# Kernel tuning notes

Measured on AMD Instinct MI355X. Metric: run time of the kernel, lower is better.

The kernel has to match this reference:

```python
import jax, jax.numpy as jnp
import numpy as np

EMBED = 128
N_RBF = 8


def setup_inputs() -> dict:
    key = jax.random.key(0)
    ks = jax.random.split(key, 12)
    n_edges = 640000
    num_atoms = 10000
    s = 1.0 / np.sqrt(EMBED)
    inp = {
        "m_ji": jax.random.normal(ks[0], (n_edges, EMBED), dtype=jnp.float32),
        "e_rbf": jax.random.normal(ks[1], (n_edges, N_RBF), dtype=jnp.float32),
        "nbr_list": jax.random.randint(ks[2], (n_edges, 2), 0, num_atoms, dtype=jnp.int32),
        "num_atoms": num_atoms,
        # params (torch Linear stores W as [out, in]; we keep that convention)
        "W_edge": jax.random.normal(ks[3], (EMBED, N_RBF), dtype=jnp.float32) / np.sqrt(N_RBF),
        "W1": jax.random.normal(ks[4], (EMBED, EMBED), dtype=jnp.float32) * s,
        "b1": jnp.zeros((EMBED,), dtype=jnp.float32),
        "W2": jax.random.normal(ks[5], (EMBED, EMBED), dtype=jnp.float32) * s,
        "b2": jnp.zeros((EMBED,), dtype=jnp.float32),
        "W3": jax.random.normal(ks[6], (EMBED, EMBED), dtype=jnp.float32) * s,
        "b3": jnp.zeros((EMBED,), dtype=jnp.float32),
        "W_final": jax.random.normal(ks[7], (EMBED, EMBED), dtype=jnp.float32) * s,
    }
    return inp


def reference(m_ji, e_rbf, nbr_list, num_atoms, W_edge, W1, b1, W2, b2, W3, b3, W_final):
    # edge_linear(e_rbf) * m_ji  -> [n_edges, embed]
    prod = (e_rbf @ W_edge.T) * m_ji
    # scatter_add over receiving atom index -> [num_atoms, embed]
    node_feats = jax.ops.segment_sum(prod, nbr_list[:, 0], num_segments=num_atoms)
    # 3 dense layers with swish (SiLU) activation
    for W, b in ((W1, b1), (W2, b2), (W3, b3)):
        node_feats = jax.nn.silu(node_feats @ W.T + b)
    # final linear (no bias)
    return node_feats @ W_final.T
```

## Files before the change

kernel.cpp:

```cpp
#include <hip/hip_runtime.h>

#define EMBED 128
#define NRBF 8
#define CAP 160

typedef __attribute__((ext_vector_type(8))) short bf16x8;
typedef __attribute__((ext_vector_type(4))) float f32x4;

static __device__ __forceinline__ unsigned short f2bf(float f) {
  unsigned u = __builtin_bit_cast(unsigned, f);
  u = (u + 0x7fffu + ((u >> 16) & 1u)) >> 16;
  return (unsigned short)u;
}

static __device__ __forceinline__ float silu_f(float x) {
  return x / (1.0f + __expf(-x));
}

__global__ __launch_bounds__(256) void prep_kernel(
    const float* __restrict__ W1, const float* __restrict__ W2,
    const float* __restrict__ W3, const float* __restrict__ Wf,
    const float* __restrict__ b1, const float* __restrict__ b2,
    const float* __restrict__ b3,
    unsigned short* __restrict__ Wbf, float* __restrict__ bws,
    unsigned* __restrict__ cursor, int num_atoms)
{
  int i = blockIdx.x * 256 + threadIdx.x;
  if (i < 16384) {
    Wbf[i]         = f2bf(W1[i]);
    Wbf[16384 + i] = f2bf(W2[i]);
    Wbf[32768 + i] = f2bf(W3[i]);
    Wbf[49152 + i] = f2bf(Wf[i]);
  }
  if (i < 128) {
    bws[i] = b1[i]; bws[128 + i] = b2[i]; bws[256 + i] = b3[i];
  }
  if (i < num_atoms) cursor[i] = 0u;
}

__global__ __launch_bounds__(256) void bucket_kernel(
    const int* __restrict__ nbr, unsigned* __restrict__ cursor,
    int* __restrict__ sorted, int n_edges)
{
  int i = blockIdx.x * blockDim.x + threadIdx.x;
  const int stride = gridDim.x * blockDim.x;
  const int2* nb = reinterpret_cast<const int2*>(nbr);
  for (; i < n_edges; i += stride) {
    const int dst = nb[i].x;
    unsigned pos = atomicAdd(&cursor[dst], 1u);
    if (pos < CAP) sorted[(size_t)dst * CAP + pos] = i;
  }
}

__global__ __launch_bounds__(256) void gather_kernel(
    const float* __restrict__ m_ji, const float* __restrict__ e_rbf,
    const int* __restrict__ sorted, const unsigned* __restrict__ cnts,
    const float* __restrict__ W_edge, unsigned short* __restrict__ node_bf,
    int num_atoms)
{
  const int lane = threadIdx.x & 63;
  const int li = lane & 31;
  const int half = lane >> 5;
  const int wid = blockIdx.x * (blockDim.x >> 6) + (threadIdx.x >> 6);
  if (wid >= num_atoms) return;

  f32x4 wT[NRBF];
#pragma unroll
  for (int k = 0; k < NRBF; ++k) {
#pragma unroll
    for (int q = 0; q < 4; ++q) wT[k][q] = W_edge[(li * 4 + q) * NRBF + k];
  }

  int cnt = (int)cnts[wid];
  if (cnt > CAP) cnt = CAP;
  const int* sb = sorted + (size_t)wid * CAP;
  const char* mbase = (const char*)m_ji;
  const char* rbase = (const char*)e_rbf;
  const unsigned moff_lane = (unsigned)(li * 16);

  f32x4 acc = {0.f, 0.f, 0.f, 0.f};

  for (int base = 0; base < cnt; base += 64) {
    const int rem = min(64, cnt - base);
    const int myeid = (base + lane < cnt) ? sb[base + lane] : sb[base];
#pragma unroll 4
    for (int j = 0; j < rem; j += 2) {
      const int idx = j + half;
      const float vm = (idx < rem) ? 1.0f : 0.0f;
      const int eid = __shfl(myeid, idx & 63);
      const unsigned mo = ((unsigned)eid << 9) + moff_lane;
      const unsigned ro = (unsigned)eid << 5;
      const f32x4 m4 = *reinterpret_cast<const f32x4*>(mbase + mo);
      const f32x4 r0 = *reinterpret_cast<const f32x4*>(rbase + ro);
      const f32x4 r1 = *reinterpret_cast<const f32x4*>(rbase + ro + 16);

      f32x4 p = wT[0] * r0.x;
      p += wT[1] * r0.y;
      p += wT[2] * r0.z;
      p += wT[3] * r0.w;
      p += wT[4] * r1.x;
      p += wT[5] * r1.y;
      p += wT[6] * r1.z;
      p += wT[7] * r1.w;
      p *= vm;
      acc += p * m4;
    }
  }

  acc[0] += __shfl_xor(acc[0], 32);
  acc[1] += __shfl_xor(acc[1], 32);
  acc[2] += __shfl_xor(acc[2], 32);
  acc[3] += __shfl_xor(acc[3], 32);

  if (half == 0) {
    unsigned u0 = (unsigned)f2bf(acc[0]) | ((unsigned)f2bf(acc[1]) << 16);
    unsigned u1 = (unsigned)f2bf(acc[2]) | ((unsigned)f2bf(acc[3]) << 16);
    uint2 v = {u0, u1};
    *reinterpret_cast<uint2*>(node_bf + (size_t)wid * EMBED + li * 4) = v;
  }
}

__global__ __launch_bounds__(256) void mlp_mfma_kernel(
    const unsigned short* __restrict__ node_bf,
    const unsigned short* __restrict__ Wbf,
    const float* __restrict__ bws,
    float* __restrict__ out, int num_atoms)
{
  __shared__ unsigned short x_lds[64 * 128];
  char* xb = (char*)x_lds;
  const int lane = threadIdx.x & 63;
  const int wave = threadIdx.x >> 6;
  const int rbase = blockIdx.x * 64;

#pragma unroll
  for (int it = 0; it < 4; ++it) {
    int i = it * 64 + lane;
    int r = i >> 4;
    int s = i & 15;
    int row = wave * 16 + r;
    int grow = rbase + row;
    uint4 v = {0u, 0u, 0u, 0u};
    if (grow < num_atoms)
      v = *reinterpret_cast<const uint4*>(node_bf + (size_t)grow * 128 + s * 8);
    *reinterpret_cast<uint4*>(xb + row * 256 + ((s ^ (row & 7)) * 16)) = v;
  }

  const int arow = wave * 16 + (lane & 15);
  const int kb = lane >> 4;
  const int colbase = lane & 15;

  f32x4 acc[8];
#pragma unroll
  for (int layer = 0; layer < 4; ++layer) {
    const unsigned short* W = Wbf + layer * 16384;
#pragma unroll
    for (int t = 0; t < 8; ++t) {
      if (layer < 3) {
        float bv = bws[layer * 128 + t * 16 + colbase];
        acc[t] = (f32x4){bv, bv, bv, bv};
      } else {
        acc[t] = (f32x4){0.f, 0.f, 0.f, 0.f};
      }
    }
#pragma unroll
    for (int ks = 0; ks < 4; ++ks) {
      bf16x8 a = *reinterpret_cast<const bf16x8*>(
          xb + arow * 256 + (((ks * 4 + kb) ^ (arow & 7)) * 16));
#pragma unroll
      for (int t = 0; t < 8; ++t) {
        int col = t * 16 + colbase;
        bf16x8 b = *reinterpret_cast<const bf16x8*>(W + col * 128 + ks * 32 + kb * 8);
        acc[t] = __builtin_amdgcn_mfma_f32_16x16x32_bf16(a, b, acc[t], 0, 0, 0);
      }
    }
    if (layer < 3) {
#pragma unroll
      for (int t = 0; t < 8; ++t) {
        int col = t * 16 + colbase;
        int s = col >> 3;
        int cw = (col & 7) * 2;
#pragma unroll
        for (int j = 0; j < 4; ++j) {
          int row = wave * 16 + (lane >> 4) * 4 + j;
          unsigned short h = f2bf(silu_f(acc[t][j]));
          *reinterpret_cast<unsigned short*>(
              xb + row * 256 + ((s ^ (row & 7)) * 16) + cw) = h;
        }
      }
    } else {
#pragma unroll
      for (int t = 0; t < 8; ++t) {
        int col = t * 16 + colbase;
#pragma unroll
        for (int j = 0; j < 4; ++j) {
          int row = wave * 16 + (lane >> 4) * 4 + j;
          int grow = rbase + row;
          if (grow < num_atoms) out[(size_t)grow * 128 + col] = acc[t][j];
        }
      }
    }
  }
}

extern "C" void kernel_launch(void* const* d_in, const int* in_sizes, int n_in,
                              void* d_out, int out_size, void* d_ws, size_t ws_size,
                              hipStream_t stream) {
  const float* m_ji   = (const float*)d_in[0];
  const float* e_rbf  = (const float*)d_in[1];
  const int*   nbr    = (const int*)d_in[2];
  const float* W_edge = (const float*)d_in[4];
  const float* W1 = (const float*)d_in[5];
  const float* b1 = (const float*)d_in[6];
  const float* W2 = (const float*)d_in[7];
  const float* b2 = (const float*)d_in[8];
  const float* W3 = (const float*)d_in[9];
  const float* b3 = (const float*)d_in[10];
  const float* Wf = (const float*)d_in[11];
  float* out = (float*)d_out;

  const int n_edges   = in_sizes[0] / EMBED;
  const int num_atoms = out_size / EMBED;

  auto align256 = [](size_t x) { return (x + 255) & ~(size_t)255; };
  char* p = (char*)d_ws;
  unsigned short* node_bf = (unsigned short*)p;
  p += align256((size_t)num_atoms * EMBED * sizeof(unsigned short));
  unsigned* cursor    = (unsigned*)p;  p += align256((size_t)num_atoms * 4);
  int* sorted         = (int*)p;       p += align256((size_t)num_atoms * CAP * 4);
  unsigned short* Wbf = (unsigned short*)p; p += align256((size_t)4 * 128 * 128 * 2);
  float* bws          = (float*)p;     p += align256((size_t)3 * 128 * 4);

  prep_kernel<<<64, 256, 0, stream>>>(W1, W2, W3, Wf, b1, b2, b3, Wbf, bws,
                                      cursor, num_atoms);

  bucket_kernel<<<1024, 256, 0, stream>>>(nbr, cursor, sorted, n_edges);

  const int gblocks = (num_atoms + 3) / 4;
  gather_kernel<<<gblocks, 256, 0, stream>>>(m_ji, e_rbf, sorted, cursor,
                                             W_edge, node_bf, num_atoms);

  const int mlp_blocks = (num_atoms + 63) / 64;
  mlp_mfma_kernel<<<mlp_blocks, 256, 0, stream>>>(node_bf, Wbf, bws, out, num_atoms);
}
```

Before: 154.7 us.

## Stream edges coalesced into per-atom bf16 payload buckets, then reduce per atom

Replaces the index-bucketing plus random gather of m_ji rows with a kernel that reads edges sequentially, computes the edge product, and writes it as bf16 into a per-destination slot claimed by atomicAdd. A second kernel reduces each atom's bucket into node features. The aim is to turn scattered 512-byte row gathers into coalesced streaming reads. In exchange it writes and rereads an intermediate of about 200 MB of bf16 workspace, quantizes each edge product to bf16 before summation, and falls back to the old path when the workspace is too small.

After: 175.4 us. 1.13x slower.

```diff
diff --git a/kernel.cpp b/kernel.cpp
--- a/kernel.cpp
+++ b/kernel.cpp
@@ -38,6 +38,96 @@
   if (i < num_atoms) cursor[i] = 0u;
 }
 
+__global__ __launch_bounds__(256) void edge_stream_kernel(
+    const float* __restrict__ m_ji, const float* __restrict__ e_rbf,
+    const int* __restrict__ nbr, const float* __restrict__ W_edge,
+    unsigned* __restrict__ cursor, unsigned short* __restrict__ payload,
+    int n_edges)
+{
+  const int lane = threadIdx.x & 63;
+  const int li = lane & 31;
+  const int half = lane >> 5;
+  const int wid = blockIdx.x * (blockDim.x >> 6) + (threadIdx.x >> 6);
+  const int n_waves = gridDim.x * (blockDim.x >> 6);
+
+  f32x4 wT[NRBF];
+#pragma unroll
+  for (int k = 0; k < NRBF; ++k) {
+#pragma unroll
+    for (int q = 0; q < 4; ++q) wT[k][q] = W_edge[(li * 4 + q) * NRBF + k];
+  }
+
+  for (int e0 = wid * 2; e0 < n_edges; e0 += n_waves * 2) {
+    const int e = e0 + half;
+    const bool act = (e < n_edges);
+    f32x4 m4 = {0.f, 0.f, 0.f, 0.f};
+    if (act) m4 = reinterpret_cast<const f32x4*>(m_ji)[(size_t)e0 * 32 + lane];
+    f32x4 r0 = {0.f, 0.f, 0.f, 0.f}, r1 = r0;
+    int dst = 0;
+    if (act) {
+      r0 = reinterpret_cast<const f32x4*>(e_rbf)[(size_t)e * 2];
+      r1 = reinterpret_cast<const f32x4*>(e_rbf)[(size_t)e * 2 + 1];
+      dst = nbr[2 * e];
+    }
+    int pos = 0;
+    if (li == 0 && act) pos = (int)atomicAdd(&cursor[dst], 1u);
+    pos = __shfl(pos, lane & 32);
+
+    f32x4 p = wT[0] * r0.x;
+    p += wT[1] * r0.y;
+    p += wT[2] * r0.z;
+    p += wT[3] * r0.w;
+    p += wT[4] * r1.x;
+    p += wT[5] * r1.y;
+    p += wT[6] * r1.z;
+    p += wT[7] * r1.w;
+    p *= m4;
+
+    if (act && pos < CAP) {
+      unsigned u0 = (unsigned)f2bf(p[0]) | ((unsigned)f2bf(p[1]) << 16);
+      unsigned u1 = (unsigned)f2bf(p[2]) | ((unsigned)f2bf(p[3]) << 16);
+      char* rowp = (char*)payload + ((size_t)dst * CAP + pos) * 256 + li * 8;
+      *reinterpret_cast<uint2*>(rowp) = (uint2){u0, u1};
+    }
+  }
+}
+
+__global__ __launch_bounds__(256) void reduce_kernel(
+    const unsigned short* __restrict__ payload,
+    const unsigned* __restrict__ cnts,
+    unsigned short* __restrict__ node_bf, int num_atoms)
+{
+  const int lane = threadIdx.x & 63;
+  const int wid = blockIdx.x * (blockDim.x >> 6) + (threadIdx.x >> 6);
+  if (wid >= num_atoms) return;
+
+  int cnt = (int)cnts[wid];
+  if (cnt > CAP) cnt = CAP;
+  const unsigned* base =
+      reinterpret_cast<const unsigned*>(payload + (size_t)wid * CAP * 128) + lane;
+
+  float a0 = 0.f, a1 = 0.f;
+  int r = 0;
+  for (; r + 8 <= cnt; r += 8) {
+    unsigned u[8];
+#pragma unroll
+    for (int k = 0; k < 8; ++k) u[k] = base[(r + k) * 64];
+#pragma unroll
+    for (int k = 0; k < 8; ++k) {
+      a0 += __builtin_bit_cast(float, u[k] << 16);
+      a1 += __builtin_bit_cast(float, u[k] & 0xffff0000u);
+    }
+  }
+  for (; r < cnt; ++r) {
+    unsigned u = base[r * 64];
+    a0 += __builtin_bit_cast(float, u << 16);
+    a1 += __builtin_bit_cast(float, u & 0xffff0000u);
+  }
+
+  unsigned pack = (unsigned)f2bf(a0) | ((unsigned)f2bf(a1) << 16);
+  *(reinterpret_cast<unsigned*>(node_bf + (size_t)wid * EMBED) + lane) = pack;
+}
+
 __global__ __launch_bounds__(256) void bucket_kernel(
     const int* __restrict__ nbr, unsigned* __restrict__ cursor,
     int* __restrict__ sorted, int n_edges)
@@ -79,7 +169,6 @@
   const unsigned moff_lane = (unsigned)(li * 16);
 
   f32x4 acc = {0.f, 0.f, 0.f, 0.f};
-
   for (int base = 0; base < cnt; base += 64) {
     const int rem = min(64, cnt - base);
     const int myeid = (base + lane < cnt) ? sb[base + lane] : sb[base];
@@ -93,7 +182,6 @@
       const f32x4 m4 = *reinterpret_cast<const f32x4*>(mbase + mo);
       const f32x4 r0 = *reinterpret_cast<const f32x4*>(rbase + ro);
       const f32x4 r1 = *reinterpret_cast<const f32x4*>(rbase + ro + 16);
-
       f32x4 p = wT[0] * r0.x;
       p += wT[1] * r0.y;
       p += wT[2] * r0.z;
@@ -106,12 +194,10 @@
       acc += p * m4;
     }
   }
-
   acc[0] += __shfl_xor(acc[0], 32);
   acc[1] += __shfl_xor(acc[1], 32);
   acc[2] += __shfl_xor(acc[2], 32);
   acc[3] += __shfl_xor(acc[3], 32);
-
   if (half == 0) {
     unsigned u0 = (unsigned)f2bf(acc[0]) | ((unsigned)f2bf(acc[1]) << 16);
     unsigned u1 = (unsigned)f2bf(acc[2]) | ((unsigned)f2bf(acc[3]) << 16);
@@ -226,18 +312,30 @@
   unsigned short* node_bf = (unsigned short*)p;
   p += align256((size_t)num_atoms * EMBED * sizeof(unsigned short));
   unsigned* cursor    = (unsigned*)p;  p += align256((size_t)num_atoms * 4);
-  int* sorted         = (int*)p;       p += align256((size_t)num_atoms * CAP * 4);
   unsigned short* Wbf = (unsigned short*)p; p += align256((size_t)4 * 128 * 128 * 2);
   float* bws          = (float*)p;     p += align256((size_t)3 * 128 * 4);
-
-  prep_kernel<<<64, 256, 0, stream>>>(W1, W2, W3, Wf, b1, b2, b3, Wbf, bws,
-                                      cursor, num_atoms);
-
-  bucket_kernel<<<1024, 256, 0, stream>>>(nbr, cursor, sorted, n_edges);
-
-  const int gblocks = (num_atoms + 3) / 4;
-  gather_kernel<<<gblocks, 256, 0, stream>>>(m_ji, e_rbf, sorted, cursor,
-                                             W_edge, node_bf, num_atoms);
+  char* tail = p;
+  const size_t payload_bytes = (size_t)num_atoms * CAP * 256;
+  const size_t need_new = (size_t)(tail - (char*)d_ws) + payload_bytes;
+
+  const int prep_blocks = (num_atoms > 16384 ? (num_atoms + 255) / 256 : 64);
+  prep_kernel<<<prep_blocks, 256, 0, stream>>>(W1, W2, W3, Wf, b1, b2, b3,
+                                               Wbf, bws, cursor, num_atoms);
+
+  if (ws_size >= need_new) {
+    unsigned short* payload = (unsigned short*)tail;
+    edge_stream_kernel<<<2048, 256, 0, stream>>>(m_ji, e_rbf, nbr, W_edge,
+                                                 cursor, payload, n_edges);
+    const int rblocks = (num_atoms + 3) / 4;
+    reduce_kernel<<<rblocks, 256, 0, stream>>>(payload, cursor, node_bf,
+                                               num_atoms);
+  } else {
+    int* sorted = (int*)tail;
+    bucket_kernel<<<1024, 256, 0, stream>>>(nbr, cursor, sorted, n_edges);
+    const int gblocks = (num_atoms + 3) / 4;
+    gather_kernel<<<gblocks, 256, 0, stream>>>(m_ji, e_rbf, sorted, cursor,
+                                               W_edge, node_bf, num_atoms);
+  }
 
   const int mlp_blocks = (num_atoms + 63) / 64;
   mlp_mfma_kernel<<<mlp_blocks, 256, 0, stream>>>(node_bf, Wbf, bws, out, num_atoms);
```
